# Kernel optimization log

Measured on AMD Instinct MI355X. Metric: run time of the kernel, lower is better.

## Reference

```python
import jax, jax.numpy as jnp
import numpy as np

M, N, D, P = 16, 4096, 128, 8192
H = N // D


def setup_inputs() -> dict:
    key = jax.random.key(0)
    ks = jax.random.split(key, 6)
    s = 1.0 / np.sqrt(N)
    return {
        "X": jax.random.normal(ks[0], (M, N), dtype=jnp.float32),
        "W_q": jax.random.normal(ks[1], (N, N), dtype=jnp.float32) * s,
        "W_k": jax.random.normal(ks[2], (N, N), dtype=jnp.float32) * s,
        "W_v": jax.random.normal(ks[3], (N, N), dtype=jnp.float32) * s,
        "cache_K": jax.random.normal(ks[4], (H, P, D), dtype=jnp.float32),
        "cache_V": jax.random.normal(ks[5], (H, P, D), dtype=jnp.float32),
    }


def reference(X, W_q, W_k, W_v, cache_K, cache_V):
    m = X.shape[0]
    h, p, d = cache_K.shape
    # QKV projections: [M, N] @ [N, N] -> [M, H, D] -> [H, M, D]
    q = (X @ W_q).reshape(m, h, d).transpose(1, 0, 2)
    k = (X @ W_k).reshape(m, h, d).transpose(1, 0, 2)
    v = (X @ W_v).reshape(m, h, d).transpose(1, 0, 2)
    # KV-cache concat along the sequence axis -> [H, P+M, D]
    k_all = jnp.concatenate([cache_K, k], axis=1)
    v_all = jnp.concatenate([cache_V, v], axis=1)
    # attention (note: original applies NO 1/sqrt(D) scaling)
    scores = jnp.einsum('hmd,hpd->hmp', q, k_all)  # [H, M, P+M]
    weights = jax.nn.softmax(scores, axis=-1)
    out = jnp.einsum('hmp,hpd->hmd', weights, v_all)  # [H, M, D]
    return out.transpose(1, 0, 2).reshape(m, h * d)
```

## Files before the change

### kernel.cpp

```cpp
#include <hip/hip_runtime.h>

#define HN 32
#define MM 16
#define DD 128
#define NN 4096
#define PP 8192
#define TP 64
#define NCH 24
#define CLEN 342
#define NTILE ((CLEN + TP - 1) / TP)

__global__ __launch_bounds__(256) void qkv_kernel(
    const float* __restrict__ X, const float* __restrict__ Wq,
    const float* __restrict__ Wk, const float* __restrict__ Wv,
    float* __restrict__ qkv)
{
    __shared__ float Xs[MM][128];
    const int bx  = blockIdx.x;
    const int mat = bx >> 8;
    const int r   = bx & 255;
    const int ct  = r >> 5;
    const int rc  = r & 31;
    const int col0 = ct << 9;
    const int i0   = rc << 7;
    const float* W = (mat == 0) ? Wq : (mat == 1) ? Wk : Wv;
    const int t = threadIdx.x;

    for (int f = t; f < MM*128; f += 256)
        Xs[f >> 7][f & 127] = X[(f >> 7)*NN + i0 + (f & 127)];
    __syncthreads();

    const int c0 = col0 + t, c1 = col0 + 256 + t;
    float a0[MM], a1[MM];
#pragma unroll
    for (int m = 0; m < MM; ++m) { a0[m] = 0.f; a1[m] = 0.f; }

    for (int i16 = 0; i16 < 128; i16 += 16) {
        const float* Wr = W + (size_t)(i0 + i16) * NN;
        float w0[16], w1[16];
#pragma unroll
        for (int rr = 0; rr < 16; ++rr) {
            w0[rr] = Wr[(size_t)rr*NN + c0];
            w1[rr] = Wr[(size_t)rr*NN + c1];
        }
#pragma unroll
        for (int m = 0; m < MM; ++m) {
            float4 xa = *reinterpret_cast<const float4*>(&Xs[m][i16]);
            float4 xb = *reinterpret_cast<const float4*>(&Xs[m][i16 + 4]);
            float4 xc = *reinterpret_cast<const float4*>(&Xs[m][i16 + 8]);
            float4 xd = *reinterpret_cast<const float4*>(&Xs[m][i16 + 12]);
            a0[m] += xa.x*w0[0] + xa.y*w0[1] + xa.z*w0[2] + xa.w*w0[3]
                   + xb.x*w0[4] + xb.y*w0[5] + xb.z*w0[6] + xb.w*w0[7]
                   + xc.x*w0[8] + xc.y*w0[9] + xc.z*w0[10] + xc.w*w0[11]
                   + xd.x*w0[12] + xd.y*w0[13] + xd.z*w0[14] + xd.w*w0[15];
            a1[m] += xa.x*w1[0] + xa.y*w1[1] + xa.z*w1[2] + xa.w*w1[3]
                   + xb.x*w1[4] + xb.y*w1[5] + xb.z*w1[6] + xb.w*w1[7]
                   + xc.x*w1[8] + xc.y*w1[9] + xc.z*w1[10] + xc.w*w1[11]
                   + xd.x*w1[12] + xd.y*w1[13] + xd.z*w1[14] + xd.w*w1[15];
        }
    }
    float* base = qkv + (size_t)mat * HN*MM*DD;
    const int h0 = c0 >> 7, d0 = c0 & 127;
    const int h1 = c1 >> 7, d1 = c1 & 127;
#pragma unroll
    for (int m = 0; m < MM; ++m) {
        atomicAdd(&base[(h0*MM + m)*DD + d0], a0[m]);
        atomicAdd(&base[(h1*MM + m)*DD + d1], a1[m]);
    }
}

__global__ __launch_bounds__(256, 3) void attn_partial4(
    const float* __restrict__ cacheK, const float* __restrict__ cacheV,
    const float* __restrict__ qkv, float* __restrict__ pmu,
    float* __restrict__ ps, float* __restrict__ pacc)
{
    __shared__ float KV[TP][DD + 4];
    __shared__ float Qs[MM][DD + 4];
    __shared__ float Wl[TP][20];

    const int chunk = blockIdx.x;
    const int h     = blockIdx.y;
    const int t     = threadIdx.x;
    const int lane  = t & 63;
    const int wv    = __builtin_amdgcn_readfirstlane((int)(threadIdx.x >> 6));
    const int srow0 = t >> 5;
    const int sg    = t & 31;
    const int psi   = lane >> 4;
    const int g     = lane & 15;

    const float* k_ws = qkv + HN*MM*DD;
    const float* v_ws = qkv + 2*HN*MM*DD;
    const int start = chunk * CLEN;

    for (int f = t; f < MM*32; f += 256) {
        const int row = f >> 5, c4 = f & 31;
        *reinterpret_cast<float4*>(&Qs[row][c4*4]) =
            *reinterpret_cast<const float4*>(qkv + ((size_t)h*MM + row)*DD + c4*4);
    }

    float mu0 = -3.0e38f, mu1 = -3.0e38f, mu2 = -3.0e38f, mu3 = -3.0e38f;
    float ss0 = 0.f, ss1 = 0.f, ss2 = 0.f, ss3 = 0.f;
    float acc[4][8];
#pragma unroll
    for (int q = 0; q < 4; ++q)
#pragma unroll
        for (int k = 0; k < 8; ++k) acc[q][k] = 0.f;

    float4 stK[8], stV[8];

    auto issueK = [&](int tt2) {
#pragma unroll
        for (int rr = 0; rr < 8; ++rr) {
            const int vr = start + tt2*TP + srow0 + 8*rr;
            float4 v = make_float4(0.f, 0.f, 0.f, 0.f);
            if (vr < PP)
                v = *reinterpret_cast<const float4*>(cacheK + ((size_t)h*PP + vr)*DD + sg*4);
            else if (vr < PP + MM)
                v = *reinterpret_cast<const float4*>(k_ws + ((size_t)h*MM + (vr - PP))*DD + sg*4);
            stK[rr] = v;
        }
    };
    auto issueV = [&](int tt2) {
#pragma unroll
        for (int rr = 0; rr < 8; ++rr) {
            const int vr = start + tt2*TP + srow0 + 8*rr;
            float4 v = make_float4(0.f, 0.f, 0.f, 0.f);
            if (vr < PP)
                v = *reinterpret_cast<const float4*>(cacheV + ((size_t)h*PP + vr)*DD + sg*4);
            else if (vr < PP + MM)
                v = *reinterpret_cast<const float4*>(v_ws + ((size_t)h*MM + (vr - PP))*DD + sg*4);
            stV[rr] = v;
        }
    };

    issueK(0);

    const float* Q0 = &Qs[4*wv + 0][0];
    const float* Q1 = &Qs[4*wv + 1][0];
    const float* Q2 = &Qs[4*wv + 2][0];
    const float* Q3 = &Qs[4*wv + 3][0];

    for (int tt = 0; tt < NTILE; ++tt) {
        const int valid = min(TP, CLEN - tt*TP);

        __syncthreads();
#pragma unroll
        for (int rr = 0; rr < 8; ++rr)
            *reinterpret_cast<float4*>(&KV[srow0 + 8*rr][sg*4]) = stK[rr];

        issueV(tt);

        __syncthreads();

        float s0 = 0.f, s1 = 0.f, s2 = 0.f, s3 = 0.f;
#pragma unroll 8
        for (int dq = 0; dq < 32; ++dq) {
            float4 k  = *reinterpret_cast<const float4*>(&KV[lane][dq*4]);
            float4 q0 = *reinterpret_cast<const float4*>(Q0 + dq*4);
            float4 q1 = *reinterpret_cast<const float4*>(Q1 + dq*4);
            float4 q2 = *reinterpret_cast<const float4*>(Q2 + dq*4);
            float4 q3 = *reinterpret_cast<const float4*>(Q3 + dq*4);
            s0 += k.x*q0.x + k.y*q0.y + k.z*q0.z + k.w*q0.w;
            s1 += k.x*q1.x + k.y*q1.y + k.z*q1.z + k.w*q1.w;
            s2 += k.x*q2.x + k.y*q2.y + k.z*q2.z + k.w*q2.w;
            s3 += k.x*q3.x + k.y*q3.y + k.z*q3.z + k.w*q3.w;
        }
        if (lane >= valid) { s0 = s1 = s2 = s3 = -3.0e38f; }

        __syncthreads();
#pragma unroll
        for (int rr = 0; rr < 8; ++rr)
            *reinterpret_cast<float4*>(&KV[srow0 + 8*rr][sg*4]) = stV[rr];

        if (tt + 1 < NTILE) issueK(tt + 1);

        float m0 = s0, m1 = s1, m2 = s2, m3 = s3;
#pragma unroll
        for (int off = 1; off < 64; off <<= 1) {
            m0 = fmaxf(m0, __shfl_xor(m0, off));
            m1 = fmaxf(m1, __shfl_xor(m1, off));
            m2 = fmaxf(m2, __shfl_xor(m2, off));
            m3 = fmaxf(m3, __shfl_xor(m3, off));
        }
        const float n0 = fmaxf(mu0, m0), n1 = fmaxf(mu1, m1);
        const float n2 = fmaxf(mu2, m2), n3 = fmaxf(mu3, m3);
        const float r0 = __expf(mu0 - n0), r1 = __expf(mu1 - n1);
        const float r2_ = __expf(mu2 - n2), r3 = __expf(mu3 - n3);
        float w0 = (lane < valid) ? __expf(s0 - n0) : 0.f;
        float w1 = (lane < valid) ? __expf(s1 - n1) : 0.f;
        float w2 = (lane < valid) ? __expf(s2 - n2) : 0.f;
        float w3 = (lane < valid) ? __expf(s3 - n3) : 0.f;
        float t0s = w0, t1s = w1, t2s = w2, t3s = w3;
#pragma unroll
        for (int off = 1; off < 64; off <<= 1) {
            t0s += __shfl_xor(t0s, off);
            t1s += __shfl_xor(t1s, off);
            t2s += __shfl_xor(t2s, off);
            t3s += __shfl_xor(t3s, off);
        }
        ss0 = ss0*r0 + t0s; ss1 = ss1*r1 + t1s;
        ss2 = ss2*r2_ + t2s; ss3 = ss3*r3 + t3s;
        mu0 = n0; mu1 = n1; mu2 = n2; mu3 = n3;
        *reinterpret_cast<float4*>(&Wl[lane][4*wv]) = make_float4(w0, w1, w2, w3);

        __syncthreads();

#pragma unroll
        for (int k = 0; k < 8; ++k) {
            acc[0][k] *= r0; acc[1][k] *= r1; acc[2][k] *= r2_; acc[3][k] *= r3;
        }
#pragma unroll 4
        for (int i = 0; i < 16; ++i) {
            const int p = psi + 4*i;
            float4 wq = *reinterpret_cast<const float4*>(&Wl[p][4*wv]);
            float4 v0 = *reinterpret_cast<const float4*>(&KV[p][g*8]);
            float4 v1 = *reinterpret_cast<const float4*>(&KV[p][g*8 + 4]);
            acc[0][0] += wq.x*v0.x; acc[0][1] += wq.x*v0.y; acc[0][2] += wq.x*v0.z; acc[0][3] += wq.x*v0.w;
            acc[0][4] += wq.x*v1.x; acc[0][5] += wq.x*v1.y; acc[0][6] += wq.x*v1.z; acc[0][7] += wq.x*v1.w;
            acc[1][0] += wq.y*v0.x; acc[1][1] += wq.y*v0.y; acc[1][2] += wq.y*v0.z; acc[1][3] += wq.y*v0.w;
            acc[1][4] += wq.y*v1.x; acc[1][5] += wq.y*v1.y; acc[1][6] += wq.y*v1.z; acc[1][7] += wq.y*v1.w;
            acc[2][0] += wq.z*v0.x; acc[2][1] += wq.z*v0.y; acc[2][2] += wq.z*v0.z; acc[2][3] += wq.z*v0.w;
            acc[2][4] += wq.z*v1.x; acc[2][5] += wq.z*v1.y; acc[2][6] += wq.z*v1.z; acc[2][7] += wq.z*v1.w;
            acc[3][0] += wq.w*v0.x; acc[3][1] += wq.w*v0.y; acc[3][2] += wq.w*v0.z; acc[3][3] += wq.w*v0.w;
            acc[3][4] += wq.w*v1.x; acc[3][5] += wq.w*v1.y; acc[3][6] += wq.w*v1.z; acc[3][7] += wq.w*v1.w;
        }
    }

#pragma unroll
    for (int q = 0; q < 4; ++q)
#pragma unroll
        for (int k = 0; k < 8; ++k) {
            float v = acc[q][k];
            v += __shfl_xor(v, 16);
            v += __shfl_xor(v, 32);
            acc[q][k] = v;
        }
    if (psi == 0) {
        float* pa = pacc + ((size_t)(h*NCH + chunk)*MM + 4*wv)*DD;
#pragma unroll
        for (int q = 0; q < 4; ++q) {
            *reinterpret_cast<float4*>(pa + q*DD + g*8) =
                make_float4(acc[q][0], acc[q][1], acc[q][2], acc[q][3]);
            *reinterpret_cast<float4*>(pa + q*DD + g*8 + 4) =
                make_float4(acc[q][4], acc[q][5], acc[q][6], acc[q][7]);
        }
    }
    if (lane == 0) {
        const int o = (h*NCH + chunk)*MM + 4*wv;
        pmu[o + 0] = mu0; pmu[o + 1] = mu1; pmu[o + 2] = mu2; pmu[o + 3] = mu3;
        ps [o + 0] = ss0; ps [o + 1] = ss1; ps [o + 2] = ss2; ps [o + 3] = ss3;
    }
}

__global__ __launch_bounds__(128) void combine_kernel(
    const float* __restrict__ pmu, const float* __restrict__ ps,
    const float* __restrict__ pacc, float* __restrict__ out)
{
    const int b = blockIdx.x;
    const int h = b >> 4, m = b & 15;
    const int d = threadIdx.x;
    float gm = -3.0e38f;
#pragma unroll
    for (int c = 0; c < NCH; ++c)
        gm = fmaxf(gm, pmu[(h*NCH + c)*MM + m]);
    float stot = 0.f, a = 0.f;
#pragma unroll
    for (int c = 0; c < NCH; ++c) {
        const float f = __expf(pmu[(h*NCH + c)*MM + m] - gm);
        stot += ps[(h*NCH + c)*MM + m] * f;
        a += pacc[((size_t)(h*NCH + c)*MM + m)*DD + d] * f;
    }
    out[m*NN + h*DD + d] = a / stot;
}

extern "C" void kernel_launch(void* const* d_in, const int* in_sizes, int n_in,
                              void* d_out, int out_size, void* d_ws, size_t ws_size,
                              hipStream_t stream) {
    const float* X  = (const float*)d_in[0];
    const float* Wq = (const float*)d_in[1];
    const float* Wk = (const float*)d_in[2];
    const float* Wv = (const float*)d_in[3];
    const float* cK = (const float*)d_in[4];
    const float* cV = (const float*)d_in[5];
    float* out = (float*)d_out;

    float* ws     = (float*)d_ws;
    float* qkv    = ws;
    float* pmu_p  = ws + 3*HN*MM*DD;
    float* ps_p   = pmu_p + HN*NCH*MM;
    float* pacc_p = ps_p + HN*NCH*MM;

    hipMemsetAsync(qkv, 0, (size_t)3*HN*MM*DD*sizeof(float), stream);
    qkv_kernel<<<768, 256, 0, stream>>>(X, Wq, Wk, Wv, qkv);
    attn_partial4<<<dim3(NCH, HN), 256, 0, stream>>>(cK, cV, qkv, pmu_p, ps_p, pacc_p);
    combine_kernel<<<HN*MM, 128, 0, stream>>>(pmu_p, ps_p, pacc_p, out);
}
```

Measured before the change: 197.7 us.

## Halve attention tile size, double chunks, drop register prefetch and Q staging

The attention kernel now uses 32-row tiles and 48 sequence chunks per head instead of 64-row tiles and 24 chunks. Each wave computes two query rows per half-wave rather than four per lane. Q is read directly from global memory instead of being staged in shared memory, and the K/V register double-buffering is replaced by direct load-then-store. Together with a higher occupancy hint, this aims to raise the number of blocks and waves in flight to hide memory latency. The trade-offs are losing the explicit load/compute overlap, doubling the partial results the combine kernel must merge, and a smaller unroll step in the QKV projection.

```diff
diff --git a/kernel.cpp b/kernel.cpp
--- a/kernel.cpp
+++ b/kernel.cpp
@@ -5,10 +5,10 @@
 #define DD 128
 #define NN 4096
 #define PP 8192
-#define TP 64
-#define NCH 24
-#define CLEN 342
-#define NTILE ((CLEN + TP - 1) / TP)
+#define TP 32
+#define NCH 48
+#define CLEN 171
+#define NTILE 6
 
 __global__ __launch_bounds__(256) void qkv_kernel(
     const float* __restrict__ X, const float* __restrict__ Wq,
@@ -35,28 +35,22 @@
 #pragma unroll
     for (int m = 0; m < MM; ++m) { a0[m] = 0.f; a1[m] = 0.f; }
 
-    for (int i16 = 0; i16 < 128; i16 += 16) {
-        const float* Wr = W + (size_t)(i0 + i16) * NN;
-        float w0[16], w1[16];
-#pragma unroll
-        for (int rr = 0; rr < 16; ++rr) {
+    for (int i8 = 0; i8 < 128; i8 += 8) {
+        const float* Wr = W + (size_t)(i0 + i8) * NN;
+        float w0[8], w1[8];
+#pragma unroll
+        for (int rr = 0; rr < 8; ++rr) {
             w0[rr] = Wr[(size_t)rr*NN + c0];
             w1[rr] = Wr[(size_t)rr*NN + c1];
         }
 #pragma unroll
         for (int m = 0; m < MM; ++m) {
-            float4 xa = *reinterpret_cast<const float4*>(&Xs[m][i16]);
-            float4 xb = *reinterpret_cast<const float4*>(&Xs[m][i16 + 4]);
-            float4 xc = *reinterpret_cast<const float4*>(&Xs[m][i16 + 8]);
-            float4 xd = *reinterpret_cast<const float4*>(&Xs[m][i16 + 12]);
+            float4 xa = *reinterpret_cast<const float4*>(&Xs[m][i8]);
+            float4 xb = *reinterpret_cast<const float4*>(&Xs[m][i8 + 4]);
             a0[m] += xa.x*w0[0] + xa.y*w0[1] + xa.z*w0[2] + xa.w*w0[3]
-                   + xb.x*w0[4] + xb.y*w0[5] + xb.z*w0[6] + xb.w*w0[7]
-                   + xc.x*w0[8] + xc.y*w0[9] + xc.z*w0[10] + xc.w*w0[11]
-                   + xd.x*w0[12] + xd.y*w0[13] + xd.z*w0[14] + xd.w*w0[15];
+                   + xb.x*w0[4] + xb.y*w0[5] + xb.z*w0[6] + xb.w*w0[7];
             a1[m] += xa.x*w1[0] + xa.y*w1[1] + xa.z*w1[2] + xa.w*w1[3]
-                   + xb.x*w1[4] + xb.y*w1[5] + xb.z*w1[6] + xb.w*w1[7]
-                   + xc.x*w1[8] + xc.y*w1[9] + xc.z*w1[10] + xc.w*w1[11]
-                   + xd.x*w1[12] + xd.y*w1[13] + xd.z*w1[14] + xd.w*w1[15];
+                   + xb.x*w1[4] + xb.y*w1[5] + xb.z*w1[6] + xb.w*w1[7];
         }
     }
     float* base = qkv + (size_t)mat * HN*MM*DD;
@@ -69,13 +63,12 @@
     }
 }
 
-__global__ __launch_bounds__(256, 3) void attn_partial4(
+__global__ __launch_bounds__(256, 6) void attn_partial5(
     const float* __restrict__ cacheK, const float* __restrict__ cacheV,
     const float* __restrict__ qkv, float* __restrict__ pmu,
     float* __restrict__ ps, float* __restrict__ pacc)
 {
     __shared__ float KV[TP][DD + 4];
-    __shared__ float Qs[MM][DD + 4];
     __shared__ float Wl[TP][20];
 
     const int chunk = blockIdx.x;
@@ -83,20 +76,18 @@
     const int t     = threadIdx.x;
     const int lane  = t & 63;
     const int wv    = __builtin_amdgcn_readfirstlane((int)(threadIdx.x >> 6));
-    const int srow0 = t >> 5;
-    const int sg    = t & 31;
+    const int hf    = lane >> 5;
+    const int p     = lane & 31;
+    const int srow  = t >> 3;
+    const int sg    = t & 7;
     const int psi   = lane >> 4;
     const int g     = lane & 15;
 
     const float* k_ws = qkv + HN*MM*DD;
     const float* v_ws = qkv + 2*HN*MM*DD;
     const int start = chunk * CLEN;
-
-    for (int f = t; f < MM*32; f += 256) {
-        const int row = f >> 5, c4 = f & 31;
-        *reinterpret_cast<float4*>(&Qs[row][c4*4]) =
-            *reinterpret_cast<const float4*>(qkv + ((size_t)h*MM + row)*DD + c4*4);
-    }
+    const float* qA = qkv + ((size_t)h*MM + 4*wv + 2*hf)*DD;
+    const float* qB = qA + DD;
 
     float mu0 = -3.0e38f, mu1 = -3.0e38f, mu2 = -3.0e38f, mu3 = -3.0e38f;
     float ss0 = 0.f, ss1 = 0.f, ss2 = 0.f, ss3 = 0.f;
@@ -106,115 +97,91 @@
 #pragma unroll
         for (int k = 0; k < 8; ++k) acc[q][k] = 0.f;
 
-    float4 stK[8], stV[8];
-
-    auto issueK = [&](int tt2) {
-#pragma unroll
-        for (int rr = 0; rr < 8; ++rr) {
-            const int vr = start + tt2*TP + srow0 + 8*rr;
-            float4 v = make_float4(0.f, 0.f, 0.f, 0.f);
-            if (vr < PP)
-                v = *reinterpret_cast<const float4*>(cacheK + ((size_t)h*PP + vr)*DD + sg*4);
-            else if (vr < PP + MM)
-                v = *reinterpret_cast<const float4*>(k_ws + ((size_t)h*MM + (vr - PP))*DD + sg*4);
-            stK[rr] = v;
-        }
-    };
-    auto issueV = [&](int tt2) {
-#pragma unroll
-        for (int rr = 0; rr < 8; ++rr) {
-            const int vr = start + tt2*TP + srow0 + 8*rr;
-            float4 v = make_float4(0.f, 0.f, 0.f, 0.f);
-            if (vr < PP)
-                v = *reinterpret_cast<const float4*>(cacheV + ((size_t)h*PP + vr)*DD + sg*4);
-            else if (vr < PP + MM)
-                v = *reinterpret_cast<const float4*>(v_ws + ((size_t)h*MM + (vr - PP))*DD + sg*4);
-            stV[rr] = v;
-        }
-    };
-
-    issueK(0);
-
-    const float* Q0 = &Qs[4*wv + 0][0];
-    const float* Q1 = &Qs[4*wv + 1][0];
-    const float* Q2 = &Qs[4*wv + 2][0];
-    const float* Q3 = &Qs[4*wv + 3][0];
-
     for (int tt = 0; tt < NTILE; ++tt) {
         const int valid = min(TP, CLEN - tt*TP);
-
-        __syncthreads();
-#pragma unroll
-        for (int rr = 0; rr < 8; ++rr)
-            *reinterpret_cast<float4*>(&KV[srow0 + 8*rr][sg*4]) = stK[rr];
-
-        issueV(tt);
-
-        __syncthreads();
-
-        float s0 = 0.f, s1 = 0.f, s2 = 0.f, s3 = 0.f;
+        const int vr    = min(start + tt*TP + srow, PP + MM - 1);
+        const float* srcK = (vr < PP) ? cacheK + ((size_t)h*PP + vr)*DD
+                                      : k_ws + ((size_t)h*MM + (vr - PP))*DD;
+        const float* srcV = (vr < PP) ? cacheV + ((size_t)h*PP + vr)*DD
+                                      : v_ws + ((size_t)h*MM + (vr - PP))*DD;
+
+        __syncthreads();
+        {
+            float4 k0 = *reinterpret_cast<const float4*>(srcK + 4*sg);
+            float4 k1 = *reinterpret_cast<const float4*>(srcK + 4*sg + 32);
+            float4 k2 = *reinterpret_cast<const float4*>(srcK + 4*sg + 64);
+            float4 k3 = *reinterpret_cast<const float4*>(srcK + 4*sg + 96);
+            *reinterpret_cast<float4*>(&KV[srow][4*sg])      = k0;
+            *reinterpret_cast<float4*>(&KV[srow][4*sg + 32]) = k1;
+            *reinterpret_cast<float4*>(&KV[srow][4*sg + 64]) = k2;
+            *reinterpret_cast<float4*>(&KV[srow][4*sg + 96]) = k3;
+        }
+        __syncthreads();
+
+        float sA = 0.f, sB = 0.f;
 #pragma unroll 8
         for (int dq = 0; dq < 32; ++dq) {
-            float4 k  = *reinterpret_cast<const float4*>(&KV[lane][dq*4]);
-            float4 q0 = *reinterpret_cast<const float4*>(Q0 + dq*4);
-            float4 q1 = *reinterpret_cast<const float4*>(Q1 + dq*4);
-            float4 q2 = *reinterpret_cast<const float4*>(Q2 + dq*4);
-            float4 q3 = *reinterpret_cast<const float4*>(Q3 + dq*4);
-            s0 += k.x*q0.x + k.y*q0.y + k.z*q0.z + k.w*q0.w;
-            s1 += k.x*q1.x + k.y*q1.y + k.z*q1.z + k.w*q1.w;
-            s2 += k.x*q2.x + k.y*q2.y + k.z*q2.z + k.w*q2.w;
-            s3 += k.x*q3.x + k.y*q3.y + k.z*q3.z + k.w*q3.w;
-        }
-        if (lane >= valid) { s0 = s1 = s2 = s3 = -3.0e38f; }
-
-        __syncthreads();
-#pragma unroll
-        for (int rr = 0; rr < 8; ++rr)
-            *reinterpret_cast<float4*>(&KV[srow0 + 8*rr][sg*4]) = stV[rr];
-
-        if (tt + 1 < NTILE) issueK(tt + 1);
-
-        float m0 = s0, m1 = s1, m2 = s2, m3 = s3;
-#pragma unroll
-        for (int off = 1; off < 64; off <<= 1) {
-            m0 = fmaxf(m0, __shfl_xor(m0, off));
-            m1 = fmaxf(m1, __shfl_xor(m1, off));
-            m2 = fmaxf(m2, __shfl_xor(m2, off));
-            m3 = fmaxf(m3, __shfl_xor(m3, off));
-        }
+            float4 k = *reinterpret_cast<const float4*>(&KV[p][dq*4]);
+            float4 a = *reinterpret_cast<const float4*>(qA + dq*4);
+            float4 b = *reinterpret_cast<const float4*>(qB + dq*4);
+            sA += k.x*a.x + k.y*a.y + k.z*a.z + k.w*a.w;
+            sB += k.x*b.x + k.y*b.y + k.z*b.z + k.w*b.w;
+        }
+        if (p >= valid) { sA = -3.0e38f; sB = -3.0e38f; }
+
+        __syncthreads();
+        {
+            float4 v0 = *reinterpret_cast<const float4*>(srcV + 4*sg);
+            float4 v1 = *reinterpret_cast<const float4*>(srcV + 4*sg + 32);
+            float4 v2 = *reinterpret_cast<const float4*>(srcV + 4*sg + 64);
+            float4 v3 = *reinterpret_cast<const float4*>(srcV + 4*sg + 96);
+            *reinterpret_cast<float4*>(&KV[srow][4*sg])      = v0;
+            *reinterpret_cast<float4*>(&KV[srow][4*sg + 32]) = v1;
+            *reinterpret_cast<float4*>(&KV[srow][4*sg + 64]) = v2;
+            *reinterpret_cast<float4*>(&KV[srow][4*sg + 96]) = v3;
+        }
+
+        float mA = sA, mB = sB;
+#pragma unroll
+        for (int off = 1; off < 32; off <<= 1) {
+            mA = fmaxf(mA, __shfl_xor(mA, off));
+            mB = fmaxf(mB, __shfl_xor(mB, off));
+        }
+        const float mAo = __shfl_xor(mA, 32), mBo = __shfl_xor(mB, 32);
+        const float m0 = hf ? mAo : mA, m1 = hf ? mBo : mB;
+        const float m2 = hf ? mA : mAo, m3 = hf ? mB : mBo;
         const float n0 = fmaxf(mu0, m0), n1 = fmaxf(mu1, m1);
         const float n2 = fmaxf(mu2, m2), n3 = fmaxf(mu3, m3);
         const float r0 = __expf(mu0 - n0), r1 = __expf(mu1 - n1);
-        const float r2_ = __expf(mu2 - n2), r3 = __expf(mu3 - n3);
-        float w0 = (lane < valid) ? __expf(s0 - n0) : 0.f;
-        float w1 = (lane < valid) ? __expf(s1 - n1) : 0.f;
-        float w2 = (lane < valid) ? __expf(s2 - n2) : 0.f;
-        float w3 = (lane < valid) ? __expf(s3 - n3) : 0.f;
-        float t0s = w0, t1s = w1, t2s = w2, t3s = w3;
-#pragma unroll
-        for (int off = 1; off < 64; off <<= 1) {
-            t0s += __shfl_xor(t0s, off);
-            t1s += __shfl_xor(t1s, off);
-            t2s += __shfl_xor(t2s, off);
-            t3s += __shfl_xor(t3s, off);
-        }
-        ss0 = ss0*r0 + t0s; ss1 = ss1*r1 + t1s;
-        ss2 = ss2*r2_ + t2s; ss3 = ss3*r3 + t3s;
+        const float r2 = __expf(mu2 - n2), r3 = __expf(mu3 - n3);
+        const float wA = __expf(sA - (hf ? n2 : n0));
+        const float wB = __expf(sB - (hf ? n3 : n1));
+        float tA = wA, tB = wB;
+#pragma unroll
+        for (int off = 1; off < 32; off <<= 1) {
+            tA += __shfl_xor(tA, off);
+            tB += __shfl_xor(tB, off);
+        }
+        const float tAo = __shfl_xor(tA, 32), tBo = __shfl_xor(tB, 32);
+        ss0 = ss0*r0 + (hf ? tAo : tA);
+        ss1 = ss1*r1 + (hf ? tBo : tB);
+        ss2 = ss2*r2 + (hf ? tA : tAo);
+        ss3 = ss3*r3 + (hf ? tB : tBo);
         mu0 = n0; mu1 = n1; mu2 = n2; mu3 = n3;
-        *reinterpret_cast<float4*>(&Wl[lane][4*wv]) = make_float4(w0, w1, w2, w3);
+        *reinterpret_cast<float2*>(&Wl[p][4*wv + 2*hf]) = make_float2(wA, wB);
 
         __syncthreads();
 
 #pragma unroll
         for (int k = 0; k < 8; ++k) {
-            acc[0][k] *= r0; acc[1][k] *= r1; acc[2][k] *= r2_; acc[3][k] *= r3;
-        }
-#pragma unroll 4
-        for (int i = 0; i < 16; ++i) {
-            const int p = psi + 4*i;
-            float4 wq = *reinterpret_cast<const float4*>(&Wl[p][4*wv]);
-            float4 v0 = *reinterpret_cast<const float4*>(&KV[p][g*8]);
-            float4 v1 = *reinterpret_cast<const float4*>(&KV[p][g*8 + 4]);
+            acc[0][k] *= r0; acc[1][k] *= r1; acc[2][k] *= r2; acc[3][k] *= r3;
+        }
+#pragma unroll
+        for (int i = 0; i < 8; ++i) {
+            const int pp = psi + 4*i;
+            float4 wq = *reinterpret_cast<const float4*>(&Wl[pp][4*wv]);
+            float4 v0 = *reinterpret_cast<const float4*>(&KV[pp][g*8]);
+            float4 v1 = *reinterpret_cast<const float4*>(&KV[pp][g*8 + 4]);
             acc[0][0] += wq.x*v0.x; acc[0][1] += wq.x*v0.y; acc[0][2] += wq.x*v0.z; acc[0][3] += wq.x*v0.w;
             acc[0][4] += wq.x*v1.x; acc[0][5] += wq.x*v1.y; acc[0][6] += wq.x*v1.z; acc[0][7] += wq.x*v1.w;
             acc[1][0] += wq.y*v0.x; acc[1][1] += wq.y*v0.y; acc[1][2] += wq.y*v0.z; acc[1][3] += wq.y*v0.w;
@@ -235,7 +202,7 @@
             v += __shfl_xor(v, 32);
             acc[q][k] = v;
         }
-    if (psi == 0) {
+    if (psi == 0 && lane < 16) {
         float* pa = pacc + ((size_t)(h*NCH + chunk)*MM + 4*wv)*DD;
 #pragma unroll
         for (int q = 0; q < 4; ++q) {
@@ -260,11 +227,11 @@
     const int h = b >> 4, m = b & 15;
     const int d = threadIdx.x;
     float gm = -3.0e38f;
-#pragma unroll
+#pragma unroll 8
     for (int c = 0; c < NCH; ++c)
         gm = fmaxf(gm, pmu[(h*NCH + c)*MM + m]);
     float stot = 0.f, a = 0.f;
-#pragma unroll
+#pragma unroll 8
     for (int c = 0; c < NCH; ++c) {
         const float f = __expf(pmu[(h*NCH + c)*MM + m] - gm);
         stot += ps[(h*NCH + c)*MM + m] * f;
@@ -292,6 +259,6 @@
 
     hipMemsetAsync(qkv, 0, (size_t)3*HN*MM*DD*sizeof(float), stream);
     qkv_kernel<<<768, 256, 0, stream>>>(X, Wq, Wk, Wv, qkv);
-    attn_partial4<<<dim3(NCH, HN), 256, 0, stream>>>(cK, cV, qkv, pmu_p, ps_p, pacc_p);
+    attn_partial5<<<dim3(NCH, HN), 256, 0, stream>>>(cK, cV, qkv, pmu_p, ps_p, pacc_p);
     combine_kernel<<<HN*MM, 128, 0, stream>>>(pmu_p, ps_p, pacc_p, out);
 }
```

After: 313.7 us. 58.7% more time.
